# Kernel optimization log

Hardware: AMD Instinct MI355X
Metric: run time of the kernel (lower is better)

The kernel has to match this reference:

```python
import jax, jax.numpy as jnp
import numpy as np

B, S, H, NH = 2, 2048, 2048, 16
HD = H // NH

def setup_inputs() -> dict:
    key = jax.random.key(0)
    ks = jax.random.split(key, 6)
    scale = 1.0 / np.sqrt(H)
    return {
        "x": jax.random.normal(ks[0], (B, S, H), dtype=jnp.float32),
        "Wq": jax.random.normal(ks[1], (H, H), dtype=jnp.float32) * scale,
        "Wk": jax.random.normal(ks[2], (H, H), dtype=jnp.float32) * scale,
        "Wv": jax.random.normal(ks[3], (H, H), dtype=jnp.float32) * scale,
        "Wo": jax.random.normal(ks[4], (H, H), dtype=jnp.float32) * scale,
        "bo": jax.random.normal(ks[5], (H,), dtype=jnp.float32) * 0.01,
    }

def reference(x, Wq, Wk, Wv, Wo, bo):
    # nn.Linear convention: y = x @ W.T (W is [out, in])
    q = (x @ Wq.T).reshape(B, S, NH, HD).transpose(0, 2, 1, 3)  # [B,NH,S,HD]
    k = (x @ Wk.T).reshape(B, S, NH, HD).transpose(0, 2, 1, 3)
    v = (x @ Wv.T).reshape(B, S, NH, HD).transpose(0, 2, 1, 3)
    scale = jnp.asarray(HD, x.dtype) ** -0.5
    scores = jnp.einsum('bhqd,bhkd->bhqk', q, k) * scale  # [B,NH,S,S]
    attn = jax.nn.softmax(scores, axis=-1)
    out = jnp.einsum('bhqk,bhkd->bhqd', attn, v)  # [B,NH,S,HD]
    out = out.transpose(0, 2, 1, 3).reshape(B, S, H)
    return out @ Wo.T + bo
```

## Files before the change

kernel.cpp:

```cpp
#include <hip/hip_runtime.h>
#include <hip/hip_bf16.h>
#include <stdint.h>

#define S_LEN 2048
#define NHEADS 16
#define HDIM 128
#define H_TOT 2048
#define BATCH 2
#define M_TOK 4096
#define KDIM 2048

typedef __attribute__((ext_vector_type(8))) short bf16x8;
typedef __attribute__((ext_vector_type(4))) float f32x4;
typedef __attribute__((ext_vector_type(16))) float f32x16;

__device__ inline ushort bf16rn(float f) {
  union { float f; uint32_t u; } x; x.f = f;
  uint32_t r = x.u + 0x7FFF + ((x.u >> 16) & 1);
  return (ushort)(r >> 16);
}

__global__ __launch_bounds__(256) void cvt5_bf16_kernel(const float* __restrict__ x,
                                                        const float* __restrict__ w0,
                                                        const float* __restrict__ w1,
                                                        const float* __restrict__ w2,
                                                        const float* __restrict__ w3,
                                                        ushort* __restrict__ xo,
                                                        ushort* __restrict__ o0,
                                                        ushort* __restrict__ o1,
                                                        ushort* __restrict__ o2,
                                                        ushort* __restrict__ o3) {
  const int NX4 = M_TOK * KDIM / 4;
  const int NW4 = KDIM * KDIM / 4;
  int i = blockIdx.x * blockDim.x + threadIdx.x;
  int stride = gridDim.x * blockDim.x;
  for (; i < NX4 + 4 * NW4; i += stride) {
    const float* in;
    ushort* out;
    int off;
    if (i < NX4) {
      in = x; out = xo; off = i;
    } else {
      int j = i - NX4;
      int seg = j >> 20;
      off = j & (NW4 - 1);
      in = (seg == 0) ? w0 : (seg == 1) ? w1 : (seg == 2) ? w2 : w3;
      out = (seg == 0) ? o0 : (seg == 1) ? o1 : (seg == 2) ? o2 : o3;
    }
    float4 v = reinterpret_cast<const float4*>(in)[off];
    ushort4 o;
    o.x = bf16rn(v.x); o.y = bf16rn(v.y); o.z = bf16rn(v.z); o.w = bf16rn(v.w);
    reinterpret_cast<ushort4*>(out)[off] = o;
  }
}

template<int MODE, int NBX>
__global__ __launch_bounds__(512) void gemm2(const ushort* __restrict__ A,
                                             const ushort* __restrict__ Bw,
                                             void* __restrict__ C0,
                                             void* __restrict__ C1,
                                             void* __restrict__ C2,
                                             const float* __restrict__ bias,
                                             float scale) {
  __shared__ __attribute__((aligned(16))) char lds[3 * 49152];
  const int K = KDIM;
  const int NKT = K / 64;
  int tid = threadIdx.x;
  int wave = tid >> 6, lane = tid & 63;
  int lanelo = lane & 15, lanehi = lane >> 4;
  int wr = wave >> 2, wc = wave & 3;

  int bid = blockIdx.x;
  const int CHX = NBX / 8;
  int ii = bid >> 3;
  int bx = (bid & 7) * CHX + (ii % CHX);
  int by = ii / CHX;
  int bm = by * 128, bn = bx * 256;

  const ushort* srcA[2];
  const ushort* srcB[4];
#pragma unroll
  for (int i = 0; i < 2; i++) {
    int c = i * 512 + tid, row = c >> 3, slot = c & 7;
    srcA[i] = A + (size_t)(bm + row) * K + ((slot ^ (row & 7)) * 8);
  }
#pragma unroll
  for (int i = 0; i < 4; i++) {
    int c = i * 512 + tid, row = c >> 3, slot = c & 7;
    srcB[i] = Bw + (size_t)(bn + row) * K + ((slot ^ (row & 7)) * 8);
  }

#define STAGE(tile, buf)                                                                    \
  {                                                                                         \
    char* dA = lds + (buf) * 49152 + (size_t)tid * 16;                                      \
    char* dB = lds + (buf) * 49152 + 16384 + (size_t)tid * 16;                              \
    _Pragma("unroll") for (int i_ = 0; i_ < 2; i_++)                                        \
      __builtin_amdgcn_global_load_lds(                                                     \
          (const __attribute__((address_space(1))) void*)(srcA[i_] + (tile) * 64),          \
          (__attribute__((address_space(3))) void*)(dA + i_ * 8192), 16, 0, 0);             \
    _Pragma("unroll") for (int i_ = 0; i_ < 4; i_++)                                        \
      __builtin_amdgcn_global_load_lds(                                                     \
          (const __attribute__((address_space(1))) void*)(srcB[i_] + (tile) * 64),          \
          (__attribute__((address_space(3))) void*)(dB + i_ * 8192), 16, 0, 0);             \
  }

  f32x4 acc[4][4];
#pragma unroll
  for (int i = 0; i < 4; i++)
#pragma unroll
    for (int j = 0; j < 4; j++) acc[i][j] = (f32x4){0.f, 0.f, 0.f, 0.f};

  STAGE(0, 0);
  STAGE(1, 1);
  asm volatile("s_waitcnt vmcnt(6)" ::: "memory");
  __builtin_amdgcn_s_barrier();
  __builtin_amdgcn_sched_barrier(0);

  for (int t = 0; t < NKT; t++) {
    STAGE((t + 2) & (NKT - 1), (t + 2) % 3);

    const ushort* bufc = (const ushort*)(lds + (t % 3) * 49152);

    bf16x8 bfr[4][2];
#pragma unroll
    for (int nf = 0; nf < 4; nf++)
#pragma unroll
      for (int kh = 0; kh < 2; kh++) {
        int row = wc * 64 + nf * 16 + lanelo;
        int slot = (kh * 4 + lanehi) ^ (row & 7);
        bfr[nf][kh] = *reinterpret_cast<const bf16x8*>(&bufc[8192 + row * 64 + slot * 8]);
      }

    __builtin_amdgcn_s_setprio(1);
#pragma unroll
    for (int mf = 0; mf < 4; mf++) {
      int row = wr * 64 + mf * 16 + lanelo;
      bf16x8 af[2];
#pragma unroll
      for (int kh = 0; kh < 2; kh++) {
        int slot = (kh * 4 + lanehi) ^ (row & 7);
        af[kh] = *reinterpret_cast<const bf16x8*>(&bufc[row * 64 + slot * 8]);
      }
#pragma unroll
      for (int nf = 0; nf < 4; nf++)
#pragma unroll
        for (int kh = 0; kh < 2; kh++)
          acc[mf][nf] = __builtin_amdgcn_mfma_f32_16x16x32_bf16(af[kh], bfr[nf][kh],
                                                                acc[mf][nf], 0, 0, 0);
    }
    __builtin_amdgcn_s_setprio(0);

    asm volatile("s_waitcnt vmcnt(6)" ::: "memory");
    __builtin_amdgcn_s_barrier();
    __builtin_amdgcn_sched_barrier(0);
  }

  if (MODE == 2) {
    float* Cf = (float*)C0;
#pragma unroll
    for (int nf = 0; nf < 4; nf++) {
      int n = bn + wc * 64 + nf * 16 + lanelo;
      float bv = bias[n];
#pragma unroll
      for (int mf = 0; mf < 4; mf++)
#pragma unroll
        for (int q = 0; q < 4; q++) {
          int m = bm + wr * 64 + mf * 16 + lanehi * 4 + q;
          Cf[(size_t)m * H_TOT + n] = acc[mf][nf][q] + bv;
        }
    }
  } else {
    int seg = bn >> 11;
    ushort* dst = (seg == 0) ? (ushort*)C0 : (seg == 1) ? (ushort*)C1 : (ushort*)C2;
    float sc = (seg == 0) ? scale : 1.0f;
#pragma unroll
    for (int nf = 0; nf < 4; nf++) {
      int n = (bn & 2047) + wc * 64 + nf * 16 + lanelo;
      int h = n >> 7, d = n & 127;
#pragma unroll
      for (int mf = 0; mf < 4; mf++)
#pragma unroll
        for (int q = 0; q < 4; q++) {
          int m = bm + wr * 64 + mf * 16 + lanehi * 4 + q;
          int b = m >> 11, s = m & 2047;
          int bh = b * NHEADS + h;
          size_t idx;
          if (seg < 2) {
            idx = (((size_t)(bh * 64 + (s >> 5)) * 8 + (d >> 4)) * 64 +
                   ((d >> 3) & 1) * 32 + (s & 31)) * 8 + (d & 7);
          } else {
            int r = s & 15;
            int e = (r & 3) | ((r >> 1) & 4);
            int hi = (r >> 2) & 1;
            idx = (((size_t)(bh * 64 + (s >> 5)) * 8 + ((s >> 4) & 1) * 4 + (d >> 5)) * 64 +
                   hi * 32 + (d & 31)) * 8 + e;
          }
          dst[idx] = bf16rn(acc[mf][nf][q] * sc);
        }
    }
  }
#undef STAGE
}

__global__ __launch_bounds__(256) void attn_kernel(const ushort* __restrict__ Qf,
                                                   const ushort* __restrict__ Kf,
                                                   const ushort* __restrict__ Vf,
                                                   ushort* __restrict__ Ob) {
  __shared__ __attribute__((aligned(16))) ushort Kl[2][4096];
  __shared__ float lsinv[4][32];
  int lane = threadIdx.x & 63, wave = threadIdx.x >> 6;
  int hi = lane >> 5;

  int bid = blockIdx.x;
  int swz = (bid & 7) * 64 + (bid >> 3);
  int bh = swz >> 4, qt = swz & 15;
  int b = bh >> 4, h = bh & 15;
  int qrow0 = qt * 128 + wave * 32;

  const bf16x8* Qv = reinterpret_cast<const bf16x8*>(Qf) +
                     ((size_t)(bh * 64 + qt * 4 + wave) * 8) * 64 + lane;
  bf16x8 qf[8];
#pragma unroll
  for (int kc = 0; kc < 8; kc++) qf[kc] = Qv[kc * 64];

  f32x16 oacc[4];
#pragma unroll
  for (int d32 = 0; d32 < 4; d32++)
#pragma unroll
    for (int r = 0; r < 16; r++) oacc[d32][r] = 0.f;
  float lsum = 0.f;
  int laneoff = lane * 8;
  const bf16x8* Vv = reinterpret_cast<const bf16x8*>(Vf) + ((size_t)bh * 64 * 8) * 64 + lane;

#define STAGE(kt, bufsel)                                                                  \
  {                                                                                        \
    size_t gchunk = ((size_t)(bh * 64 + (kt))) * 8;                                        \
    _Pragma("unroll")                                                                      \
    for (int i_ = 0; i_ < 2; i_++) {                                                       \
      int cc = wave * 2 + i_;                                                              \
      __builtin_amdgcn_global_load_lds(                                                    \
          (const __attribute__((address_space(1))) void*)(Kf + (gchunk + cc) * 512 +       \
                                                          laneoff),                        \
          (__attribute__((address_space(3))) void*)(&Kl[bufsel][cc * 512]), 16, 0, 0);     \
    }                                                                                      \
  }

  union pu { bf16x8 v; uint32_t u[4]; };
  pu paA0, paA1, paB0, paB1;
  bf16x8 vrA[8], vrB[8];
  const bf16x8 bz = {0, 0, 0, 0, 0, 0, 0, 0};
#pragma unroll
  for (int j = 0; j < 4; j++) { paA0.u[j] = 0; paA1.u[j] = 0; }
#pragma unroll
  for (int i = 0; i < 8; i++) vrA[i] = bz;

  STAGE(0, 0);
  asm volatile("s_waitcnt vmcnt(0)" ::: "memory");
  __syncthreads();

  const int NT = S_LEN / 32;

#define BODY(T, PI0, PI1, VI, PO0, PO1, VO)                                                 \
  {                                                                                         \
    if ((T) + 1 < NT) STAGE((T) + 1, ((T) + 1) & 1);                                        \
    _Pragma("unroll") for (int i_ = 0; i_ < 8; i_++)                                        \
      VO[i_] = Vv[((size_t)(T) * 8 + i_) * 64];     \
    const ushort* lb = &Kl[(T) & 1][0];                                                     \
    f32x16 S;                                                                               \
    _Pragma("unroll") for (int r = 0; r < 16; r++) S[r] = 0.f;                              \
    __builtin_amdgcn_s_setprio(1);                                                          \
    _Pragma("unroll") for (int kc = 0; kc < 8; kc++) {                                      \
      bf16x8 kfr = *reinterpret_cast<const bf16x8*>(&lb[kc * 512 + laneoff]);               \
      S = __builtin_amdgcn_mfma_f32_32x32x16_bf16(kfr, qf[kc], S, 0, 0, 0);                 \
    }                                                                                       \
    _Pragma("unroll") for (int d32 = 0; d32 < 4; d32++) {                                   \
      oacc[d32] = __builtin_amdgcn_mfma_f32_32x32x16_bf16(PI0.v, VI[d32], oacc[d32], 0, 0, 0); \
      oacc[d32] = __builtin_amdgcn_mfma_f32_32x32x16_bf16(PI1.v, VI[4 + d32], oacc[d32], 0, 0, 0); \
    }                                                                                       \
    __builtin_amdgcn_s_setprio(0);                                                          \
    float p_[16];                                                                           \
    _Pragma("unroll") for (int r = 0; r < 16; r++) { p_[r] = exp2f(S[r]); lsum += p_[r]; }  \
    _Pragma("unroll") for (int j = 0; j < 4; j++) {                                         \
      uint32_t w0_, w1_;                                                                    \
      asm("v_cvt_pk_bf16_f32 %0, %1, %2" : "=v"(w0_) : "v"(p_[2 * j]), "v"(p_[2 * j + 1])); \
      asm("v_cvt_pk_bf16_f32 %0, %1, %2" : "=v"(w1_) : "v"(p_[8 + 2 * j]), "v"(p_[9 + 2 * j])); \
      PO0.u[j] = w0_; PO1.u[j] = w1_;                                                       \
    }                                                                                       \
    asm volatile("s_waitcnt vmcnt(0)" ::: "memory");                                        \
    __syncthreads();                                                                        \
  }

  for (int t = 0; t < NT; t += 2) {
    BODY(t,     paA0, paA1, vrA, paB0, paB1, vrB);
    BODY(t + 1, paB0, paB1, vrB, paA0, paA1, vrA);
  }
#pragma unroll
  for (int d32 = 0; d32 < 4; d32++) {
    oacc[d32] = __builtin_amdgcn_mfma_f32_32x32x16_bf16(paA0.v, vrA[d32], oacc[d32], 0, 0, 0);
    oacc[d32] = __builtin_amdgcn_mfma_f32_32x32x16_bf16(paA1.v, vrA[4 + d32], oacc[d32], 0, 0, 0);
  }

  float total = lsum + __shfl_xor(lsum, 32);
  if (lane < 32) lsinv[wave][lane] = 1.0f / total;
  __syncthreads();

  float ls[16];
#pragma unroll
  for (int r = 0; r < 16; r++) ls[r] = lsinv[wave][(r & 3) + 8 * (r >> 2) + 4 * hi];
#pragma unroll
  for (int d32 = 0; d32 < 4; d32++)
#pragma unroll
    for (int r = 0; r < 16; r++) {
      int row = (r & 3) + 8 * (r >> 2) + 4 * hi;
      size_t idx = ((size_t)(b * S_LEN + qrow0 + row)) * H_TOT + h * HDIM + d32 * 32 + (lane & 31);
      Ob[idx] = bf16rn(oacc[d32][r] * ls[r]);
    }
#undef BODY
#undef STAGE
}

extern "C" void kernel_launch(void* const* d_in, const int* in_sizes, int n_in,
                              void* d_out, int out_size, void* d_ws, size_t ws_size,
                              hipStream_t stream) {
  const float* x  = (const float*)d_in[0];
  const float* Wq = (const float*)d_in[1];
  const float* Wk = (const float*)d_in[2];
  const float* Wv = (const float*)d_in[3];
  const float* Wo = (const float*)d_in[4];
  const float* bo = (const float*)d_in[5];
  float* out = (float*)d_out;

  char* w = (char*)d_ws;
  ushort* xb  = (ushort*)w; w += (size_t)M_TOK * KDIM * 2;
  ushort* Wqb = (ushort*)w; w += (size_t)KDIM * KDIM * 2;
  ushort* Wkb = (ushort*)w; w += (size_t)KDIM * KDIM * 2;
  ushort* Wvb = (ushort*)w; w += (size_t)KDIM * KDIM * 2;
  ushort* Wob = (ushort*)w; w += (size_t)KDIM * KDIM * 2;
  ushort* Qh  = (ushort*)w; w += (size_t)M_TOK * KDIM * 2;
  ushort* Kh  = (ushort*)w; w += (size_t)M_TOK * KDIM * 2;
  ushort* Vt  = (ushort*)w; w += (size_t)M_TOK * KDIM * 2;
  ushort* Ob  = (ushort*)w; w += (size_t)M_TOK * KDIM * 2;

  hipLaunchKernelGGL(cvt5_bf16_kernel, dim3(2048), dim3(256), 0, stream,
                     x, Wq, Wk, Wv, Wo, xb, Wqb, Wkb, Wvb, Wob);

  const float sl = 0.08838834764831845f * 1.4426950408889634f;

  hipLaunchKernelGGL((gemm2<0, 24>), dim3(768), dim3(512), 0, stream,
                     xb, Wqb, (void*)Qh, (void*)Kh, (void*)Vt, (const float*)nullptr, sl);

  hipLaunchKernelGGL(attn_kernel, dim3(512), dim3(256), 0, stream, Qh, Kh, Vt, Ob);

  hipLaunchKernelGGL((gemm2<2, 8>), dim3(256), dim3(512), 0, stream,
                     Ob, Wob, (void*)out, nullptr, nullptr, bo, 1.0f);
}
```

Before: 266.0 us.

## Process 64-key tiles per iteration and drop cross-iteration P·V software pipeline

The attention loop now stages 64 keys per step instead of 32, computes two QK^T score tiles that interleave their MFMAs, then applies softmax and the P·V MFMAs within the same iteration. This removes the ping-pong register pipeline that deferred P·V to the next tile and halves the number of barriers and waitcnts per key sequence. The cost is a doubled LDS K buffer and 16 V fragments live at once, which raises register pressure. It also loses the overlap between exp work and the previous tile's P·V MFMAs.

New measurement: 320.6 us. +20.5%, slower.

```diff
diff --git a/kernel.cpp b/kernel.cpp
--- a/kernel.cpp
+++ b/kernel.cpp
@@ -206,7 +206,7 @@
                                                    const ushort* __restrict__ Kf,
                                                    const ushort* __restrict__ Vf,
                                                    ushort* __restrict__ Ob) {
-  __shared__ __attribute__((aligned(16))) ushort Kl[2][4096];
+  __shared__ __attribute__((aligned(16))) ushort Kl[2][16 * 512];
   __shared__ float lsinv[4][32];
   int lane = threadIdx.x & 63, wave = threadIdx.x >> 6;
   int hi = lane >> 5;
@@ -232,12 +232,12 @@
   int laneoff = lane * 8;
   const bf16x8* Vv = reinterpret_cast<const bf16x8*>(Vf) + ((size_t)bh * 64 * 8) * 64 + lane;
 
-#define STAGE(kt, bufsel)                                                                  \
+#define STAGE(kt2, bufsel)                                                                 \
   {                                                                                        \
-    size_t gchunk = ((size_t)(bh * 64 + (kt))) * 8;                                        \
+    size_t gchunk = ((size_t)(bh * 64 + 2 * (kt2))) * 8;                                   \
     _Pragma("unroll")                                                                      \
-    for (int i_ = 0; i_ < 2; i_++) {                                                       \
-      int cc = wave * 2 + i_;                                                              \
+    for (int i_ = 0; i_ < 4; i_++) {                                                       \
+      int cc = wave * 4 + i_;                                                              \
       __builtin_amdgcn_global_load_lds(                                                    \
           (const __attribute__((address_space(1))) void*)(Kf + (gchunk + cc) * 512 +       \
                                                           laneoff),                        \
@@ -246,58 +246,65 @@
   }
 
   union pu { bf16x8 v; uint32_t u[4]; };
-  pu paA0, paA1, paB0, paB1;
-  bf16x8 vrA[8], vrB[8];
-  const bf16x8 bz = {0, 0, 0, 0, 0, 0, 0, 0};
-#pragma unroll
-  for (int j = 0; j < 4; j++) { paA0.u[j] = 0; paA1.u[j] = 0; }
-#pragma unroll
-  for (int i = 0; i < 8; i++) vrA[i] = bz;
 
   STAGE(0, 0);
   asm volatile("s_waitcnt vmcnt(0)" ::: "memory");
   __syncthreads();
 
-  const int NT = S_LEN / 32;
-
-#define BODY(T, PI0, PI1, VI, PO0, PO1, VO)                                                 \
-  {                                                                                         \
-    if ((T) + 1 < NT) STAGE((T) + 1, ((T) + 1) & 1);                                        \
-    _Pragma("unroll") for (int i_ = 0; i_ < 8; i_++)                                        \
-      VO[i_] = Vv[((size_t)(T) * 8 + i_) * 64];     \
-    const ushort* lb = &Kl[(T) & 1][0];                                                     \
-    f32x16 S;                                                                               \
-    _Pragma("unroll") for (int r = 0; r < 16; r++) S[r] = 0.f;                              \
-    __builtin_amdgcn_s_setprio(1);                                                          \
-    _Pragma("unroll") for (int kc = 0; kc < 8; kc++) {                                      \
-      bf16x8 kfr = *reinterpret_cast<const bf16x8*>(&lb[kc * 512 + laneoff]);               \
-      S = __builtin_amdgcn_mfma_f32_32x32x16_bf16(kfr, qf[kc], S, 0, 0, 0);                 \
-    }                                                                                       \
-    _Pragma("unroll") for (int d32 = 0; d32 < 4; d32++) {                                   \
-      oacc[d32] = __builtin_amdgcn_mfma_f32_32x32x16_bf16(PI0.v, VI[d32], oacc[d32], 0, 0, 0); \
-      oacc[d32] = __builtin_amdgcn_mfma_f32_32x32x16_bf16(PI1.v, VI[4 + d32], oacc[d32], 0, 0, 0); \
-    }                                                                                       \
-    __builtin_amdgcn_s_setprio(0);                                                          \
-    float p_[16];                                                                           \
-    _Pragma("unroll") for (int r = 0; r < 16; r++) { p_[r] = exp2f(S[r]); lsum += p_[r]; }  \
-    _Pragma("unroll") for (int j = 0; j < 4; j++) {                                         \
-      uint32_t w0_, w1_;                                                                    \
-      asm("v_cvt_pk_bf16_f32 %0, %1, %2" : "=v"(w0_) : "v"(p_[2 * j]), "v"(p_[2 * j + 1])); \
-      asm("v_cvt_pk_bf16_f32 %0, %1, %2" : "=v"(w1_) : "v"(p_[8 + 2 * j]), "v"(p_[9 + 2 * j])); \
-      PO0.u[j] = w0_; PO1.u[j] = w1_;                                                       \
-    }                                                                                       \
-    asm volatile("s_waitcnt vmcnt(0)" ::: "memory");                                        \
-    __syncthreads();                                                                        \
-  }
-
-  for (int t = 0; t < NT; t += 2) {
-    BODY(t,     paA0, paA1, vrA, paB0, paB1, vrB);
-    BODY(t + 1, paB0, paB1, vrB, paA0, paA1, vrA);
-  }
-#pragma unroll
-  for (int d32 = 0; d32 < 4; d32++) {
-    oacc[d32] = __builtin_amdgcn_mfma_f32_32x32x16_bf16(paA0.v, vrA[d32], oacc[d32], 0, 0, 0);
-    oacc[d32] = __builtin_amdgcn_mfma_f32_32x32x16_bf16(paA1.v, vrA[4 + d32], oacc[d32], 0, 0, 0);
+  const int NT2 = S_LEN / 64;
+
+  for (int t = 0; t < NT2; t++) {
+    if (t + 1 < NT2) STAGE(t + 1, (t + 1) & 1);
+
+    bf16x8 vr[16];
+#pragma unroll
+    for (int i = 0; i < 16; i++) vr[i] = Vv[((size_t)(2 * t) * 8 + i) * 64];
+
+    const ushort* lb = &Kl[t & 1][0];
+    f32x16 Sa, Sb;
+#pragma unroll
+    for (int r = 0; r < 16; r++) { Sa[r] = 0.f; Sb[r] = 0.f; }
+    __builtin_amdgcn_s_setprio(1);
+#pragma unroll
+    for (int kc = 0; kc < 8; kc++) {
+      bf16x8 ka = *reinterpret_cast<const bf16x8*>(&lb[kc * 512 + laneoff]);
+      bf16x8 kb = *reinterpret_cast<const bf16x8*>(&lb[(8 + kc) * 512 + laneoff]);
+      Sa = __builtin_amdgcn_mfma_f32_32x32x16_bf16(ka, qf[kc], Sa, 0, 0, 0);
+      Sb = __builtin_amdgcn_mfma_f32_32x32x16_bf16(kb, qf[kc], Sb, 0, 0, 0);
+    }
+    __builtin_amdgcn_s_setprio(0);
+
+    pu pa0, pa1, pb0, pb1;
+#pragma unroll
+    for (int j = 0; j < 4; j++) {
+      float a0 = exp2f(Sa[2 * j]), a1 = exp2f(Sa[2 * j + 1]);
+      float a2 = exp2f(Sa[8 + 2 * j]), a3 = exp2f(Sa[9 + 2 * j]);
+      lsum += (a0 + a1) + (a2 + a3);
+      uint32_t w0_, w1_;
+      asm("v_cvt_pk_bf16_f32 %0, %1, %2" : "=v"(w0_) : "v"(a0), "v"(a1));
+      asm("v_cvt_pk_bf16_f32 %0, %1, %2" : "=v"(w1_) : "v"(a2), "v"(a3));
+      pa0.u[j] = w0_; pa1.u[j] = w1_;
+      float b0 = exp2f(Sb[2 * j]), b1 = exp2f(Sb[2 * j + 1]);
+      float b2 = exp2f(Sb[8 + 2 * j]), b3 = exp2f(Sb[9 + 2 * j]);
+      lsum += (b0 + b1) + (b2 + b3);
+      uint32_t w2_, w3_;
+      asm("v_cvt_pk_bf16_f32 %0, %1, %2" : "=v"(w2_) : "v"(b0), "v"(b1));
+      asm("v_cvt_pk_bf16_f32 %0, %1, %2" : "=v"(w3_) : "v"(b2), "v"(b3));
+      pb0.u[j] = w2_; pb1.u[j] = w3_;
+    }
+
+    __builtin_amdgcn_s_setprio(1);
+#pragma unroll
+    for (int d32 = 0; d32 < 4; d32++) {
+      oacc[d32] = __builtin_amdgcn_mfma_f32_32x32x16_bf16(pa0.v, vr[d32], oacc[d32], 0, 0, 0);
+      oacc[d32] = __builtin_amdgcn_mfma_f32_32x32x16_bf16(pa1.v, vr[4 + d32], oacc[d32], 0, 0, 0);
+      oacc[d32] = __builtin_amdgcn_mfma_f32_32x32x16_bf16(pb0.v, vr[8 + d32], oacc[d32], 0, 0, 0);
+      oacc[d32] = __builtin_amdgcn_mfma_f32_32x32x16_bf16(pb1.v, vr[12 + d32], oacc[d32], 0, 0, 0);
+    }
+    __builtin_amdgcn_s_setprio(0);
+
+    asm volatile("s_waitcnt vmcnt(0)" ::: "memory");
+    __syncthreads();
   }
 
   float total = lsum + __shfl_xor(lsum, 32);
@@ -315,7 +322,6 @@
       size_t idx = ((size_t)(b * S_LEN + qrow0 + row)) * H_TOT + h * HDIM + d32 * 32 + (lane & 31);
       Ob[idx] = bf16rn(oacc[d32][r] * ls[r]);
     }
-#undef BODY
 #undef STAGE
 }
 
```
